# Kernel tuning notes

Measured on AMD Instinct MI355X. Metric: run time of the kernel, lower is better.

Reference implementation:

```python
import jax, jax.numpy as jnp
import numpy as np

B, T, HS = 2, 2048, 4096
H, HK, D = 32, 8, 128  # num_heads, num_kv_heads, head_dim; HS == H*D
N_REP = H // HK


def setup_inputs() -> dict:
    key = jax.random.key(0)
    k1, k2, k3 = jax.random.split(key, 3)
    x = jax.random.normal(k1, (B, T, HS), dtype=jnp.float32)
    # qkv Linear (no bias): out_features = HS + 2*HK*D
    W_qkv = jax.random.normal(k2, (HS + 2 * HK * D, HS), dtype=jnp.float32) * 0.02
    W_proj = jax.random.normal(k3, (HS, HS), dtype=jnp.float32) * 0.02
    # Realistic RoPE cache (rotate-half convention): [1, T, 1, D]
    pos = jnp.arange(T, dtype=jnp.float32)
    inv_freq = 1.0 / (10000.0 ** (jnp.arange(0, D, 2, dtype=jnp.float32) / D))
    ang = pos[:, None] * inv_freq[None, :]                      # [T, D/2]
    rope_cos = jnp.concatenate([jnp.cos(ang), jnp.cos(ang)], -1)[None, :, None, :]
    rope_sin = jnp.concatenate([jnp.sin(ang), jnp.sin(ang)], -1)[None, :, None, :]
    return {"x": x, "rope_cos": rope_cos, "rope_sin": rope_sin,
            "W_qkv": W_qkv, "W_proj": W_proj}


def _rotate_half(u):
    u1, u2 = jnp.split(u, 2, axis=-1)
    return jnp.concatenate([-u2, u1], axis=-1)


def _apply_rope(u, cos, sin):
    return u * cos + _rotate_half(u) * sin


def reference(x, rope_cos, rope_sin, W_qkv, W_proj):
    # fused QKV projection
    qkv = jnp.einsum('btc,oc->bto', x, W_qkv)
    q, k, v = jnp.split(qkv, [HS, HS + HK * D], axis=-1)
    q = q.reshape(B, T, H, D)
    k = k.reshape(B, T, HK, D)
    v = v.reshape(B, T, HK, D)
    # inline RoPE on q and k
    q = _apply_rope(q, rope_cos[:, :T], rope_sin[:, :T])
    k = _apply_rope(k, rope_cos[:, :T], rope_sin[:, :T])
    # GQA repeat_kv: [B,T,HK,D] -> [B,T,H,D]
    k = jnp.repeat(k, N_REP, axis=2)
    v = jnp.repeat(v, N_REP, axis=2)
    # causal attention (flash-equivalent math)
    scale = 1.0 / jnp.sqrt(jnp.asarray(D, dtype=q.dtype))
    scores = jnp.einsum('bqhd,bkhd->bhqk', q, k) * scale        # [B,H,T,T]
    causal = jnp.tril(jnp.ones((T, T), dtype=bool))
    scores = jnp.where(causal[None, None], scores, jnp.finfo(scores.dtype).min)
    p = jax.nn.softmax(scores, axis=-1)
    out = jnp.einsum('bhqk,bkhd->bqhd', p, v).reshape(B, T, HS)
    return jnp.einsum('btc,oc->bto', out, W_proj)
```

## Files before the change

kernel.cpp:

```cpp
#include <hip/hip_runtime.h>
#include <hip/hip_bf16.h>

typedef __attribute__((ext_vector_type(8))) short short8;
typedef __attribute__((ext_vector_type(4))) short short4v;
typedef __attribute__((ext_vector_type(4))) float floatx4;

__device__ __forceinline__ float b2f(ushort u) {
  unsigned x = ((unsigned)u) << 16;
  return __builtin_bit_cast(float, x);
}
__device__ __forceinline__ ushort f2b(float f) {
  unsigned x = __builtin_bit_cast(unsigned, f);
  x += 0x7fffu + ((x >> 16) & 1u);
  return (ushort)(x >> 16);
}

__device__ __forceinline__ void gload_lds16(const void* g, void* l) {
  __builtin_amdgcn_global_load_lds(
      (const __attribute__((address_space(1))) unsigned int*)g,
      (__attribute__((address_space(3))) unsigned int*)l, 16, 0, 0);
}

__global__ __launch_bounds__(256) void cvt_kernel(const float* __restrict__ in,
                                                  ushort* __restrict__ out, long n) {
  long i0 = ((long)blockIdx.x * 256 + threadIdx.x) * 4;
  long stride = (long)gridDim.x * 256 * 4;
  for (long i = i0; i < n; i += stride) {
    float4 v = *(const float4*)(in + i);
    ushort4 u;
    u.x = f2b(v.x); u.y = f2b(v.y); u.z = f2b(v.z); u.w = f2b(v.w);
    *(ushort4*)(out + i) = u;
  }
}

template <int BN, int OUTBF16>
__global__ __launch_bounds__(512, 2)
void gemm_pipe(const ushort* __restrict__ A, const ushort* __restrict__ B,
               float* __restrict__ Cf, ushort* __restrict__ Cb,
               int M, int N, int K) {
  constexpr int BNF = BN / 64;
  __shared__ __align__(16) ushort sA[2][256 * 64];
  __shared__ __align__(16) ushort sB[2][BN * 64];
  const int t = threadIdx.x;
  const int lane = t & 63;
  const int L = lane & 15, g = lane >> 4;
  const int w = t >> 6;
  const int wr = w >> 2, wc = w & 3;
  const int ntn = N / BN;
  const int nwg = gridDim.x;
  const int wg = blockIdx.x;
  const int swz = (wg & 7) * (nwg >> 3) + (wg >> 3);
  const int m0 = (swz / ntn) << 8;
  const int n0 = (swz % ntn) * BN;

  floatx4 acc[8][BNF];
#pragma unroll
  for (int i = 0; i < 8; i++)
#pragma unroll
    for (int j = 0; j < BNF; j++) acc[i][j] = (floatx4)(0.0f);

  const ushort* Ab = A + (size_t)m0 * K;
  const ushort* Bb = B + (size_t)n0 * K;

  auto stage_tile = [&](const ushort* Ag, const ushort* Bg, int buf) {
#pragma unroll
    for (int j = 0; j < 4; j++) {
      const int c = j * 512 + t;
      const int row = c >> 3, ch = c & 7;
      const int kc = ch ^ (row & 7);
      gload_lds16(Ag + (size_t)row * K + kc * 8, (char*)&sA[buf][0] + c * 16);
    }
#pragma unroll
    for (int j = 0; j < BN / 64; j++) {
      const int c = j * 512 + t;
      const int row = c >> 3, ch = c & 7;
      const int kc = ch ^ (row & 7);
      gload_lds16(Bg + (size_t)row * K + kc * 8, (char*)&sB[buf][0] + c * 16);
    }
  };
  auto rdA = [&](int buf, int mh, int kc16, short8* dst) {
#pragma unroll
    for (int i = 0; i < 4; i++) {
      const int row = wr * 128 + mh * 64 + i * 16 + L;
      const int ch = (kc16 * 4 + g) ^ (row & 7);
      dst[i] = *(const short8*)((const char*)&sA[buf][0] + row * 128 + ch * 16);
    }
  };
  auto rdB = [&](int buf, int kc16, short8* dst) {
#pragma unroll
    for (int i = 0; i < BNF; i++) {
      const int row = wc * (BN / 4) + i * 16 + L;
      const int ch = (kc16 * 4 + g) ^ (row & 7);
      dst[i] = *(const short8*)((const char*)&sB[buf][0] + row * 128 + ch * 16);
    }
  };

  short8 a0[4], a1[4], b0[BNF], b1[BNF];

  auto mfmaN = [&](short8* af, short8* bf, int accbase, int cnt) {
    __builtin_amdgcn_s_setprio(1);
    for (int i = 0; i < cnt; i++)
#pragma unroll
      for (int nf = 0; nf < BNF; nf++)
        acc[accbase + i][nf] =
            __builtin_amdgcn_mfma_f32_16x16x32_bf16(af[i], bf[nf], acc[accbase + i][nf], 0, 0, 0);
    __builtin_amdgcn_s_setprio(0);
  };

  const int NT = K >> 6;
  stage_tile(Ab, Bb, 0);
  __syncthreads();
  rdA(0, 0, 0, a0);
  rdB(0, 0, b0);

  for (int T = 0; T < NT; ++T) {
    const int p = T & 1, q = p ^ 1;
    const bool more = (T + 1 < NT);
    if (more) stage_tile(Ab + (T + 1) * 64, Bb + (T + 1) * 64, q);
    rdA(p, 1, 0, a1);
    mfmaN(a0, b0, 0, 4);
    rdA(p, 0, 1, a0);
    rdB(p, 1, b1);
    mfmaN(a1, b0, 4, 4);
    rdA(p, 1, 1, a1);
    mfmaN(a0, b1, 0, 4);
    mfmaN(a1, b1, 4, 2);
    __syncthreads();
    if (more) {
      rdA(q, 0, 0, a0);
      rdB(q, 0, b0);
    }
    mfmaN(a1 + 2, b1, 6, 2);
  }

#pragma unroll
  for (int mf = 0; mf < 8; mf++)
#pragma unroll
    for (int nf = 0; nf < BNF; nf++)
#pragma unroll
      for (int r = 0; r < 4; r++) {
        const int row = m0 + wr * 128 + mf * 16 + g * 4 + r;
        const int col = n0 + wc * (BN / 4) + nf * 16 + L;
        if (OUTBF16)
          Cb[(size_t)row * N + col] = f2b(acc[mf][nf][r]);
        else
          Cf[(size_t)row * N + col] = acc[mf][nf][r];
      }
}

__global__ __launch_bounds__(256)
void rope_kernel(const ushort* __restrict__ qkv, const float* __restrict__ cosp,
                 const float* __restrict__ sinp, ushort* __restrict__ Qo,
                 ushort* __restrict__ Ko) {
  const int row = blockIdx.x;
  const int b = row >> 11, tt = row & 2047;
  const int i = threadIdx.x;
  const ushort* qr = qkv + (size_t)row * 6144;

  const int jb = (i & 7) * 8;
  float cs[8], sn[8];
  *(float4*)&cs[0] = *(const float4*)(cosp + tt * 128 + jb);
  *(float4*)&cs[4] = *(const float4*)(cosp + tt * 128 + jb + 4);
  *(float4*)&sn[0] = *(const float4*)(sinp + tt * 128 + jb);
  *(float4*)&sn[4] = *(const float4*)(sinp + tt * 128 + jb + 4);

  {
    const int hh = i >> 3;
    short8 lo = *(const short8*)(qr + hh * 128 + jb);
    short8 hi = *(const short8*)(qr + hh * 128 + 64 + jb);
    short8 olo, ohi;
#pragma unroll
    for (int e = 0; e < 8; e++) {
      float fl = b2f((ushort)lo[e]), fh = b2f((ushort)hi[e]);
      olo[e] = (short)f2b(fl * cs[e] - fh * sn[e]);
      ohi[e] = (short)f2b(fh * cs[e] + fl * sn[e]);
    }
    ushort* dst = Qo + ((size_t)(b * 32 + hh) * 2048 + tt) * 128 + jb;
    *(short8*)dst = olo;
    *(short8*)(dst + 64) = ohi;
  }
  if (i < 64) {
    const int hkk = i >> 3;
    short8 lo = *(const short8*)(qr + 4096 + hkk * 128 + jb);
    short8 hi = *(const short8*)(qr + 4096 + hkk * 128 + 64 + jb);
    short8 olo, ohi;
#pragma unroll
    for (int e = 0; e < 8; e++) {
      float fl = b2f((ushort)lo[e]), fh = b2f((ushort)hi[e]);
      olo[e] = (short)f2b(fl * cs[e] - fh * sn[e]);
      ohi[e] = (short)f2b(fh * cs[e] + fl * sn[e]);
    }
    ushort* dst = Ko + ((size_t)(b * 8 + hkk) * 2048 + tt) * 128 + jb;
    *(short8*)dst = olo;
    *(short8*)(dst + 64) = ohi;
  }
}

__global__ __launch_bounds__(256)
void vtrans_kernel(const ushort* __restrict__ qkv, ushort* __restrict__ Vt) {
  const int bx = blockIdx.x;
  const int t0 = (bx & 31) * 64;
  const int hk = (bx >> 5) & 7;
  const int b = bx >> 8;
  const int i = threadIdx.x;
  const int tq = i & 15;
  const int dn = i >> 4;
  const ushort* src = qkv + ((size_t)(b * 2048 + t0 + tq * 4)) * 6144 + 5120 + hk * 128 + dn * 8;
  short8 v0 = *(const short8*)(src);
  short8 v1 = *(const short8*)(src + 6144);
  short8 v2 = *(const short8*)(src + 12288);
  short8 v3 = *(const short8*)(src + 18432);
  ushort* dst = Vt + ((size_t)(b * 8 + hk) * 128 + dn * 8) * 2048 + t0 + tq * 4;
#pragma unroll
  for (int e = 0; e < 8; e++) {
    short4v pk;
    pk[0] = v0[e]; pk[1] = v1[e]; pk[2] = v2[e]; pk[3] = v3[e];
    *(short4v*)(dst + (size_t)e * 2048) = pk;
  }
}

#define ATT_SCALE 0.08838834764831845f

__global__ __launch_bounds__(256, 2)
void attn_kernel(const ushort* __restrict__ Q, const ushort* __restrict__ Kg,
                 const ushort* __restrict__ Vtg, ushort* __restrict__ O) {
  __shared__ __align__(16) ushort Klds[2][64 * 128];
  __shared__ __align__(16) ushort Vlds[2][128 * 64];
  __shared__ __align__(16) ushort Plds[4][32 * 64];
  const int t = threadIdx.x, lane = t & 63, w = t >> 6;
  const int bx = blockIdx.x;
  const int hk = bx & 7;
  const int qh = (bx >> 3) & 3;
  const int b = (bx >> 5) & 1;
  const int pair = bx >> 6;
  const int h = hk * 4 + qh;
  const int qtA = pair, qtB = 15 - pair;
  const int nA = (qtA + 1) * 2, nB = (qtB + 1) * 2;
  const int total = nA + nB;

  const ushort* Qp = Q + ((size_t)(b * 32 + h) * 2048) * 128;
  const ushort* Kp = Kg + ((size_t)(b * 8 + hk) * 2048) * 128;
  const ushort* Vp = Vtg + ((size_t)(b * 8 + hk) * 128) * 2048;

  const int L = lane & 15, g = lane >> 4;

  auto stage = [&](int s) {
    const int tt = (s < nA) ? s : s - nA;
    const int kv0 = tt * 64;
    ushort* Kd = Klds[s & 1];
    ushort* Vd = Vlds[s & 1];
#pragma unroll
    for (int j = 0; j < 4; j++) {
      const int c = j * 256 + t;
      const int krow = c >> 4, kcol = c & 15;
      gload_lds16(Kp + (size_t)(kv0 + krow) * 128 + ((kcol ^ (krow & 15)) << 3),
                  (char*)Kd + c * 16);
    }
#pragma unroll
    for (int j = 0; j < 4; j++) {
      const int c = j * 256 + t;
      const int d = c >> 3, tc = c & 7;
      gload_lds16(Vp + (size_t)d * 2048 + kv0 + ((tc ^ (d & 7)) << 3),
                  (char*)Vd + c * 16);
    }
  };

  short8 qf[2][4];
  floatx4 o[2][8];
  float mrun[2][4], lrun[2][4];

  auto init_pass = [&](int qw) {
#pragma unroll
    for (int m = 0; m < 2; m++) {
#pragma unroll
      for (int kc = 0; kc < 4; kc++)
        qf[m][kc] = *(const short8*)(Qp + (size_t)(qw + m * 16 + L) * 128 + kc * 32 + g * 8);
#pragma unroll
      for (int dt = 0; dt < 8; dt++) o[m][dt] = (floatx4)(0.0f);
#pragma unroll
      for (int r = 0; r < 4; r++) { mrun[m][r] = -3.0e38f; lrun[m][r] = 0.0f; }
    }
  };

  auto compute = [&](int tt, int bsel, int qw) {
    const int kv0 = tt * 64;
    if (kv0 > qw + 31) return;
    const ushort* Kd = Klds[bsel];
    const ushort* Vd = Vlds[bsel];
    ushort* Pw = Plds[w];
    floatx4 sfr[2][4];
#pragma unroll
    for (int m = 0; m < 2; m++)
#pragma unroll
      for (int n = 0; n < 4; n++) sfr[m][n] = (floatx4)(0.0f);
#pragma unroll
    for (int kc = 0; kc < 4; kc++) {
#pragma unroll
      for (int n = 0; n < 4; n++) {
        const int krow = n * 16 + L;
        const int ck = ((kc << 2) + g) ^ L;
        short8 kf = *(const short8*)((const char*)Kd + krow * 256 + ck * 16);
        sfr[0][n] = __builtin_amdgcn_mfma_f32_16x16x32_bf16(qf[0][kc], kf, sfr[0][n], 0, 0, 0);
        sfr[1][n] = __builtin_amdgcn_mfma_f32_16x16x32_bf16(qf[1][kc], kf, sfr[1][n], 0, 0, 0);
      }
    }
    float mx[2][4];
#pragma unroll
    for (int m = 0; m < 2; m++)
#pragma unroll
      for (int r = 0; r < 4; r++) {
        const int qg = qw + m * 16 + g * 4 + r;
        float mm = -3.0e38f;
#pragma unroll
        for (int n = 0; n < 4; n++) {
          float v = sfr[m][n][r] * ATT_SCALE;
          if (kv0 + n * 16 + L > qg) v = -1e30f;
          sfr[m][n][r] = v;
          mm = fmaxf(mm, v);
        }
        mx[m][r] = mm;
      }
#pragma unroll
    for (int off = 1; off < 16; off <<= 1)
#pragma unroll
      for (int m = 0; m < 2; m++)
#pragma unroll
        for (int r = 0; r < 4; r++)
          mx[m][r] = fmaxf(mx[m][r], __shfl_xor(mx[m][r], off, 64));
    float alpha[2][4], ls[2][4];
#pragma unroll
    for (int m = 0; m < 2; m++)
#pragma unroll
      for (int r = 0; r < 4; r++) {
        float mnew = fmaxf(mrun[m][r], mx[m][r]);
        alpha[m][r] = __expf(mrun[m][r] - mnew);
        mrun[m][r] = mnew;
        ls[m][r] = 0.0f;
      }
#pragma unroll
    for (int m = 0; m < 2; m++)
#pragma unroll
      for (int n = 0; n < 4; n++)
#pragma unroll
        for (int r = 0; r < 4; r++) {
          float p = __expf(sfr[m][n][r] - mrun[m][r]);
          sfr[m][n][r] = p;
          ls[m][r] += p;
        }
#pragma unroll
    for (int off = 1; off < 16; off <<= 1)
#pragma unroll
      for (int m = 0; m < 2; m++)
#pragma unroll
        for (int r = 0; r < 4; r++)
          ls[m][r] += __shfl_xor(ls[m][r], off, 64);
#pragma unroll
    for (int m = 0; m < 2; m++)
#pragma unroll
      for (int r = 0; r < 4; r++)
        lrun[m][r] = lrun[m][r] * alpha[m][r] + ls[m][r];
#pragma unroll
    for (int m = 0; m < 2; m++)
#pragma unroll
      for (int n = 0; n < 4; n++)
#pragma unroll
        for (int r = 0; r < 4; r++) {
          const int R = m * 16 + g * 4 + r;
          const int col = n * 16 + L;
          Pw[R * 64 + (col ^ (r << 4))] = f2b(sfr[m][n][r]);
        }
#pragma unroll
    for (int m = 0; m < 2; m++)
#pragma unroll
      for (int dt = 0; dt < 8; dt++)
#pragma unroll
        for (int r = 0; r < 4; r++) o[m][dt][r] *= alpha[m][r];
#pragma unroll
    for (int kc = 0; kc < 2; kc++) {
      short8 pf[2];
#pragma unroll
      for (int m = 0; m < 2; m++) {
        const int R = m * 16 + L;
        const int C = kc * 32 + g * 8;
        pf[m] = *(const short8*)&Pw[R * 64 + (C ^ ((L & 3) << 4))];
      }
#pragma unroll
      for (int dt = 0; dt < 8; dt++) {
        const int d = dt * 16 + L;
        const int gp = ((kc << 2) + g) ^ (d & 7);
        short8 vf = *(const short8*)((const char*)Vd + d * 128 + gp * 16);
        o[0][dt] = __builtin_amdgcn_mfma_f32_16x16x32_bf16(pf[0], vf, o[0][dt], 0, 0, 0);
        o[1][dt] = __builtin_amdgcn_mfma_f32_16x16x32_bf16(pf[1], vf, o[1][dt], 0, 0, 0);
      }
    }
  };

  auto epilogue = [&](int qw) {
#pragma unroll
    for (int m = 0; m < 2; m++)
#pragma unroll
      for (int r = 0; r < 4; r++) {
        const float inv = 1.0f / lrun[m][r];
        const int qg = qw + m * 16 + g * 4 + r;
#pragma unroll
        for (int dt = 0; dt < 8; dt++)
          O[(size_t)(b * 2048 + qg) * 4096 + h * 128 + dt * 16 + L] =
              f2b(o[m][dt][r] * inv);
      }
  };

  int s = 0;
  stage(0);
  __syncthreads();

  int qw = qtA * 128 + w * 32;
  init_pass(qw);
  for (int i = 0; i < nA; ++i, ++s) {
    if (s + 1 < total) stage(s + 1);
    compute(i, s & 1, qw);
    __syncthreads();
  }
  epilogue(qw);

  qw = qtB * 128 + w * 32;
  init_pass(qw);
  for (int i = 0; i < nB; ++i, ++s) {
    if (s + 1 < total) stage(s + 1);
    compute(i, s & 1, qw);
    __syncthreads();
  }
  epilogue(qw);
}

extern "C" void kernel_launch(void* const* d_in, const int* in_sizes, int n_in,
                              void* d_out, int out_size, void* d_ws, size_t ws_size,
                              hipStream_t stream) {
  const float* x = (const float*)d_in[0];
  const float* rc = (const float*)d_in[1];
  const float* rs = (const float*)d_in[2];
  const float* wqkv = (const float*)d_in[3];
  const float* wproj = (const float*)d_in[4];
  float* out = (float*)d_out;

  ushort* xb = (ushort*)d_ws;
  ushort* wqkvb = xb + 16777216;
  ushort* qkvb = wqkvb + 25165824;
  ushort* Qb = qkvb + 25165824;
  ushort* Kb = Qb + 16777216;
  ushort* Vt = Kb + 4194304;
  ushort* wprojb = xb;
  ushort* aob = qkvb;

  cvt_kernel<<<2048, 256, 0, stream>>>(x, xb, 16777216L);
  cvt_kernel<<<2048, 256, 0, stream>>>(wqkv, wqkvb, 25165824L);
  gemm_pipe<192, 1><<<512, 512, 0, stream>>>(xb, wqkvb, nullptr, qkvb, 4096, 6144, 4096);
  rope_kernel<<<4096, 256, 0, stream>>>(qkvb, rc, rs, Qb, Kb);
  vtrans_kernel<<<512, 256, 0, stream>>>(qkvb, Vt);
  attn_kernel<<<512, 256, 0, stream>>>(Qb, Kb, Vt, aob);
  cvt_kernel<<<2048, 256, 0, stream>>>(wproj, wprojb, 16777216L);
  gemm_pipe<256, 0><<<256, 512, 0, stream>>>(aob, wprojb, out, nullptr, 4096, 4096, 4096);
}
```

Baseline: 534.8 us.

## Rewrite attention inner loop with transposed 32x32 MFMA and register-resident P

```diff
diff --git a/kernel.cpp b/kernel.cpp
--- a/kernel.cpp
+++ b/kernel.cpp
@@ -4,6 +4,8 @@
 typedef __attribute__((ext_vector_type(8))) short short8;
 typedef __attribute__((ext_vector_type(4))) short short4v;
 typedef __attribute__((ext_vector_type(4))) float floatx4;
+typedef __attribute__((ext_vector_type(16))) float floatx16;
+typedef __attribute__((ext_vector_type(4))) unsigned int uintx4;
 
 __device__ __forceinline__ float b2f(ushort u) {
   unsigned x = ((unsigned)u) << 16;
@@ -19,6 +21,26 @@
   __builtin_amdgcn_global_load_lds(
       (const __attribute__((address_space(1))) unsigned int*)g,
       (__attribute__((address_space(3))) unsigned int*)l, 16, 0, 0);
+}
+
+__device__ __forceinline__ short8 mkpa8(float p0, float p1, float p2, float p3,
+                                        float p4, float p5, float p6, float p7,
+                                        bool hi) {
+  unsigned a0, a1, b0, b1;
+  asm("v_cvt_pk_bf16_f32 %0, %1, %2" : "=v"(a0) : "v"(p0), "v"(p1));
+  asm("v_cvt_pk_bf16_f32 %0, %1, %2" : "=v"(a1) : "v"(p2), "v"(p3));
+  asm("v_cvt_pk_bf16_f32 %0, %1, %2" : "=v"(b0) : "v"(p4), "v"(p5));
+  asm("v_cvt_pk_bf16_f32 %0, %1, %2" : "=v"(b1) : "v"(p6), "v"(p7));
+  unsigned sa0 = (unsigned)__shfl_xor((int)a0, 32, 64);
+  unsigned sa1 = (unsigned)__shfl_xor((int)a1, 32, 64);
+  unsigned sb0 = (unsigned)__shfl_xor((int)b0, 32, 64);
+  unsigned sb1 = (unsigned)__shfl_xor((int)b1, 32, 64);
+  uintx4 u;
+  u[0] = hi ? sb0 : a0;
+  u[1] = hi ? sb1 : a1;
+  u[2] = hi ? b0 : sa0;
+  u[3] = hi ? b1 : sa1;
+  return __builtin_bit_cast(short8, u);
 }
 
 __global__ __launch_bounds__(256) void cvt_kernel(const float* __restrict__ in,
@@ -219,14 +241,14 @@
   }
 }
 
-#define ATT_SCALE 0.08838834764831845f
+#define ATT_C2 0.1275172707611085f
 
 __global__ __launch_bounds__(256, 2)
 void attn_kernel(const ushort* __restrict__ Q, const ushort* __restrict__ Kg,
                  const ushort* __restrict__ Vtg, ushort* __restrict__ O) {
   __shared__ __align__(16) ushort Klds[2][64 * 128];
   __shared__ __align__(16) ushort Vlds[2][128 * 64];
-  __shared__ __align__(16) ushort Plds[4][32 * 64];
+  __shared__ __align__(16) ushort Olds[4][32 * 64];
   const int t = threadIdx.x, lane = t & 63, w = t >> 6;
   const int bx = blockIdx.x;
   const int hk = bx & 7;
@@ -242,7 +264,9 @@
   const ushort* Kp = Kg + ((size_t)(b * 8 + hk) * 2048) * 128;
   const ushort* Vp = Vtg + ((size_t)(b * 8 + hk) * 128) * 2048;
 
-  const int L = lane & 15, g = lane >> 4;
+  const int l31 = lane & 31;
+  const bool hib = lane >= 32;
+  const int hi = hib ? 1 : 0;
 
   auto stage = [&](int s) {
     const int tt = (s < nA) ? s : s - nA;
@@ -265,148 +289,120 @@
     }
   };
 
-  short8 qf[2][4];
-  floatx4 o[2][8];
-  float mrun[2][4], lrun[2][4];
-
-  auto init_pass = [&](int qw) {
-#pragma unroll
-    for (int m = 0; m < 2; m++) {
-#pragma unroll
-      for (int kc = 0; kc < 4; kc++)
-        qf[m][kc] = *(const short8*)(Qp + (size_t)(qw + m * 16 + L) * 128 + kc * 32 + g * 8);
-#pragma unroll
-      for (int dt = 0; dt < 8; dt++) o[m][dt] = (floatx4)(0.0f);
-#pragma unroll
-      for (int r = 0; r < 4; r++) { mrun[m][r] = -3.0e38f; lrun[m][r] = 0.0f; }
-    }
-  };
-
-  auto compute = [&](int tt, int bsel, int qw) {
+  short8 qf[8];
+  floatx16 o[4];
+  float mrun, lrun;
+
+  auto init_pass = [&](int qw_) {
+#pragma unroll
+    for (int ks = 0; ks < 8; ks++)
+      qf[ks] = *(const short8*)(Qp + (size_t)(qw_ + l31) * 128 + ks * 16 + hi * 8);
+#pragma unroll
+    for (int d = 0; d < 4; d++) o[d] = (floatx16)(0.0f);
+    mrun = -3.0e38f;
+    lrun = 0.0f;
+  };
+
+  auto compute = [&](int tt, int bsel, int qw_) {
     const int kv0 = tt * 64;
-    if (kv0 > qw + 31) return;
+    if (kv0 > qw_ + 31) return;
     const ushort* Kd = Klds[bsel];
     const ushort* Vd = Vlds[bsel];
-    ushort* Pw = Plds[w];
-    floatx4 sfr[2][4];
-#pragma unroll
-    for (int m = 0; m < 2; m++)
-#pragma unroll
-      for (int n = 0; n < 4; n++) sfr[m][n] = (floatx4)(0.0f);
-#pragma unroll
-    for (int kc = 0; kc < 4; kc++) {
-#pragma unroll
-      for (int n = 0; n < 4; n++) {
-        const int krow = n * 16 + L;
-        const int ck = ((kc << 2) + g) ^ L;
-        short8 kf = *(const short8*)((const char*)Kd + krow * 256 + ck * 16);
-        sfr[0][n] = __builtin_amdgcn_mfma_f32_16x16x32_bf16(qf[0][kc], kf, sfr[0][n], 0, 0, 0);
-        sfr[1][n] = __builtin_amdgcn_mfma_f32_16x16x32_bf16(qf[1][kc], kf, sfr[1][n], 0, 0, 0);
+    floatx16 s0 = (floatx16)(0.0f), s1 = (floatx16)(0.0f);
+#pragma unroll
+    for (int ks = 0; ks < 8; ks++) {
+      const int gc = ks * 2 + hi;
+      const int r0 = l31;
+      short8 kf0 = *(const short8*)((const char*)Kd + r0 * 256 + ((gc ^ (r0 & 15)) * 16));
+      s0 = __builtin_amdgcn_mfma_f32_32x32x16_bf16(kf0, qf[ks], s0, 0, 0, 0);
+      const int r1 = 32 + l31;
+      short8 kf1 = *(const short8*)((const char*)Kd + r1 * 256 + ((gc ^ (r1 & 15)) * 16));
+      s1 = __builtin_amdgcn_mfma_f32_32x32x16_bf16(kf1, qf[ks], s1, 0, 0, 0);
+    }
+    const int qg = qw_ + l31;
+    if (kv0 + 63 > qw_) {
+#pragma unroll
+      for (int r = 0; r < 16; r++) {
+        const int kvr = (r & 3) + 8 * (r >> 2) + 4 * hi;
+        if (kv0 + kvr > qg) s0[r] = -3.0e38f;
+        if (kv0 + 32 + kvr > qg) s1[r] = -3.0e38f;
       }
     }
-    float mx[2][4];
-#pragma unroll
-    for (int m = 0; m < 2; m++)
-#pragma unroll
-      for (int r = 0; r < 4; r++) {
-        const int qg = qw + m * 16 + g * 4 + r;
-        float mm = -3.0e38f;
-#pragma unroll
-        for (int n = 0; n < 4; n++) {
-          float v = sfr[m][n][r] * ATT_SCALE;
-          if (kv0 + n * 16 + L > qg) v = -1e30f;
-          sfr[m][n][r] = v;
-          mm = fmaxf(mm, v);
+    float m1 = fmaxf(s0[0], s0[1]);
+#pragma unroll
+    for (int r = 2; r < 16; r++) m1 = fmaxf(m1, s0[r]);
+#pragma unroll
+    for (int r = 0; r < 16; r++) m1 = fmaxf(m1, s1[r]);
+    m1 = fmaxf(m1, __shfl_xor(m1, 32, 64));
+    if (!__all(m1 - mrun <= 62.73f)) {
+      const float mnew = fmaxf(mrun, m1);
+      const float alpha = __builtin_amdgcn_exp2f((mrun - mnew) * ATT_C2);
+      lrun *= alpha;
+#pragma unroll
+      for (int d = 0; d < 4; d++)
+#pragma unroll
+        for (int r = 0; r < 16; r++) o[d][r] *= alpha;
+      mrun = mnew;
+    }
+    float ls = 0.0f;
+#pragma unroll
+    for (int r = 0; r < 16; r++) {
+      float p = __builtin_amdgcn_exp2f((s0[r] - mrun) * ATT_C2);
+      s0[r] = p; ls += p;
+    }
+#pragma unroll
+    for (int r = 0; r < 16; r++) {
+      float p = __builtin_amdgcn_exp2f((s1[r] - mrun) * ATT_C2);
+      s1[r] = p; ls += p;
+    }
+    ls += __shfl_xor(ls, 32, 64);
+    lrun += ls;
+    short8 pa00 = mkpa8(s0[0], s0[1], s0[2], s0[3], s0[4], s0[5], s0[6], s0[7], hib);
+    short8 pa01 = mkpa8(s0[8], s0[9], s0[10], s0[11], s0[12], s0[13], s0[14], s0[15], hib);
+    short8 pa10 = mkpa8(s1[0], s1[1], s1[2], s1[3], s1[4], s1[5], s1[6], s1[7], hib);
+    short8 pa11 = mkpa8(s1[8], s1[9], s1[10], s1[11], s1[12], s1[13], s1[14], s1[15], hib);
+#pragma unroll
+    for (int kvb = 0; kvb < 2; kvb++)
+#pragma unroll
+      for (int sh = 0; sh < 2; sh++) {
+        const short8 pa = (kvb == 0) ? (sh == 0 ? pa00 : pa01) : (sh == 0 ? pa10 : pa11);
+        const int gc = kvb * 4 + sh * 2 + hi;
+#pragma unroll
+        for (int d = 0; d < 4; d++) {
+          const int vr = d * 32 + l31;
+          short8 vf = *(const short8*)((const char*)Vd + vr * 128 + ((gc ^ (vr & 7)) * 16));
+          o[d] = __builtin_amdgcn_mfma_f32_32x32x16_bf16(vf, pa, o[d], 0, 0, 0);
         }
-        mx[m][r] = mm;
       }
-#pragma unroll
-    for (int off = 1; off < 16; off <<= 1)
-#pragma unroll
-      for (int m = 0; m < 2; m++)
-#pragma unroll
-        for (int r = 0; r < 4; r++)
-          mx[m][r] = fmaxf(mx[m][r], __shfl_xor(mx[m][r], off, 64));
-    float alpha[2][4], ls[2][4];
-#pragma unroll
-    for (int m = 0; m < 2; m++)
-#pragma unroll
-      for (int r = 0; r < 4; r++) {
-        float mnew = fmaxf(mrun[m][r], mx[m][r]);
-        alpha[m][r] = __expf(mrun[m][r] - mnew);
-        mrun[m][r] = mnew;
-        ls[m][r] = 0.0f;
+  };
+
+  auto epilogue = [&](int qw_) {
+    const float inv = 1.0f / lrun;
+    ushort* Ow = Olds[w];
+    const int q = l31;
+#pragma unroll
+    for (int half = 0; half < 2; half++) {
+#pragma unroll
+      for (int dd = 0; dd < 2; dd++) {
+        const int dblk = half * 2 + dd;
+#pragma unroll
+        for (int rp = 0; rp < 8; rp++) {
+          const int r0 = rp * 2;
+          const int d0 = dd * 32 + (r0 & 3) + 8 * (r0 >> 2) + 4 * hi;
+          unsigned pk;
+          asm("v_cvt_pk_bf16_f32 %0, %1, %2" : "=v"(pk)
+              : "v"(o[dblk][r0] * inv), "v"(o[dblk][r0 + 1] * inv));
+          *(unsigned*)&Ow[q * 64 + (d0 ^ ((q & 7) << 3))] = pk;
+        }
       }
 #pragma unroll
-    for (int m = 0; m < 2; m++)
-#pragma unroll
-      for (int n = 0; n < 4; n++)
-#pragma unroll
-        for (int r = 0; r < 4; r++) {
-          float p = __expf(sfr[m][n][r] - mrun[m][r]);
-          sfr[m][n][r] = p;
-          ls[m][r] += p;
-        }
-#pragma unroll
-    for (int off = 1; off < 16; off <<= 1)
-#pragma unroll
-      for (int m = 0; m < 2; m++)
-#pragma unroll
-        for (int r = 0; r < 4; r++)
-          ls[m][r] += __shfl_xor(ls[m][r], off, 64);
-#pragma unroll
-    for (int m = 0; m < 2; m++)
-#pragma unroll
-      for (int r = 0; r < 4; r++)
-        lrun[m][r] = lrun[m][r] * alpha[m][r] + ls[m][r];
-#pragma unroll
-    for (int m = 0; m < 2; m++)
-#pragma unroll
-      for (int n = 0; n < 4; n++)
-#pragma unroll
-        for (int r = 0; r < 4; r++) {
-          const int R = m * 16 + g * 4 + r;
-          const int col = n * 16 + L;
-          Pw[R * 64 + (col ^ (r << 4))] = f2b(sfr[m][n][r]);
-        }
-#pragma unroll
-    for (int m = 0; m < 2; m++)
-#pragma unroll
-      for (int dt = 0; dt < 8; dt++)
-#pragma unroll
-        for (int r = 0; r < 4; r++) o[m][dt][r] *= alpha[m][r];
-#pragma unroll
-    for (int kc = 0; kc < 2; kc++) {
-      short8 pf[2];
-#pragma unroll
-      for (int m = 0; m < 2; m++) {
-        const int R = m * 16 + L;
-        const int C = kc * 32 + g * 8;
-        pf[m] = *(const short8*)&Pw[R * 64 + (C ^ ((L & 3) << 4))];
+      for (int qs = 0; qs < 4; qs++) {
+        const int qq = qs * 8 + (lane >> 3);
+        const int seg = lane & 7;
+        short8 v = *(const short8*)&Ow[qq * 64 + ((seg * 8) ^ ((qq & 7) << 3))];
+        *(short8*)&O[(size_t)(b * 2048 + qw_ + qq) * 4096 + h * 128 + half * 64 + seg * 8] = v;
       }
-#pragma unroll
-      for (int dt = 0; dt < 8; dt++) {
-        const int d = dt * 16 + L;
-        const int gp = ((kc << 2) + g) ^ (d & 7);
-        short8 vf = *(const short8*)((const char*)Vd + d * 128 + gp * 16);
-        o[0][dt] = __builtin_amdgcn_mfma_f32_16x16x32_bf16(pf[0], vf, o[0][dt], 0, 0, 0);
-        o[1][dt] = __builtin_amdgcn_mfma_f32_16x16x32_bf16(pf[1], vf, o[1][dt], 0, 0, 0);
-      }
-    }
-  };
-
-  auto epilogue = [&](int qw) {
-#pragma unroll
-    for (int m = 0; m < 2; m++)
-#pragma unroll
-      for (int r = 0; r < 4; r++) {
-        const float inv = 1.0f / lrun[m][r];
-        const int qg = qw + m * 16 + g * 4 + r;
-#pragma unroll
-        for (int dt = 0; dt < 8; dt++)
-          O[(size_t)(b * 2048 + qg) * 4096 + h * 128 + dt * 16 + L] =
-              f2b(o[m][dt][r] * inv);
-      }
+    }
   };
 
   int s = 0;
```

Measured after the change: 474.0 us. 11.4% less time.
